# Kernel optimization log

Hardware: AMD Instinct MI355X
Metric: run time of the kernel (lower is better)

Reference implementation:

```python
import jax, jax.numpy as jnp
import numpy as np

ATT_NORM = 4.0
EPS = 1e-12

E, H, C, N = 1000000, 8, 16, 100000


def setup_inputs() -> dict:
    key = jax.random.key(0)
    k1, k2, k3, k4, k5 = jax.random.split(key, 5)
    return {
        "x": jax.random.normal(k1, (E, H, C), dtype=jnp.float32),
        "att_l": jax.random.normal(k2, (1, H, C), dtype=jnp.float32),
        "att_r": jax.random.normal(k3, (1, H, C), dtype=jnp.float32),
        "alpha": jax.random.normal(k4, (E, H, 1), dtype=jnp.float32),
        "index": jax.random.randint(k5, (E,), 0, N, dtype=jnp.int32),
        "num_nodes": N,
    }


def reference(x, att_l, att_r, alpha, index, num_nodes):
    # squared L2 norm of per-edge features: [E, H, 1]
    norm_x = jnp.sum(x * x, axis=-1, keepdims=True)
    # scatter-max per destination node: [N, H, 1]
    max_norm_seg = jax.ops.segment_max(norm_x, index, num_segments=num_nodes)
    # gather back per edge and combine: sqrt(max_norm[index] + norm_x)
    max_norm = jnp.sqrt(max_norm_seg[index] + norm_x)  # [E, H, 1]
    # norm of concatenated attention vectors: ||[att_l, att_r]|| over last dim -> [1, H, 1]
    norm_att = ATT_NORM * jnp.sqrt(
        jnp.sum(att_l * att_l, axis=-1, keepdims=True)
        + jnp.sum(att_r * att_r, axis=-1, keepdims=True)
    )
    return alpha / (norm_att * max_norm + EPS)
```

## Files before the change

kernel.cpp:

```cpp
#include <hip/hip_runtime.h>
#include <math.h>

#define EPSF 1e-12f
#define ATT_NORM_F 4.0f
#define H_DIM 8
#define C_DIM 16
#define N_NODES 100000

__global__ __launch_bounds__(256) void lip_pass1(
    const float* __restrict__ x, const int* __restrict__ index,
    float* __restrict__ norm_x, unsigned int* __restrict__ seg, int rows)
{
    int tid = blockIdx.x * blockDim.x + threadIdx.x;
    int r = tid >> 2;
    int lane = tid & 3;
    if (r >= rows) return;

    const float4* x4 = (const float4*)x;
    float4 v = x4[(size_t)r * 4 + lane];
    float s = v.x * v.x + v.y * v.y + v.z * v.z + v.w * v.w;
    s += __shfl_xor(s, 1);
    s += __shfl_xor(s, 2);

    if (lane == 0) {
        norm_x[r] = s;
        int e = r >> 3;
        int h = r & 7;
        atomicMax(&seg[(size_t)index[e] * H_DIM + h], __float_as_uint(s));
    }
}

__global__ __launch_bounds__(256) void lip_pass2(
    const float* __restrict__ norm_x, const float* __restrict__ alpha,
    const int* __restrict__ index, const unsigned int* __restrict__ seg,
    const float* __restrict__ att_l, const float* __restrict__ att_r,
    float* __restrict__ out, int total)
{
    __shared__ float s_natt[H_DIM];
    int t = threadIdx.x;
    if (t < H_DIM) {
        float s = 0.f;
        #pragma unroll
        for (int c = 0; c < C_DIM; ++c) {
            float l = att_l[t * C_DIM + c];
            float r = att_r[t * C_DIM + c];
            s += l * l + r * r;
        }
        s_natt[t] = ATT_NORM_F * sqrtf(s);
    }
    __syncthreads();

    int tid = blockIdx.x * blockDim.x + t;
    if (tid >= total) return;

    int e    = tid >> 1;
    int half = tid & 1;
    int idx  = index[e];

    const float4* nx4 = (const float4*)norm_x;
    const float4* al4 = (const float4*)alpha;
    const float4* sg4 = (const float4*)seg;

    float4 nx = nx4[tid];
    float4 al = al4[tid];
    float4 sg = sg4[(size_t)idx * 2 + half];

    int h0 = half * 4;
    float4 o;
    o.x = al.x / (s_natt[h0 + 0] * sqrtf(sg.x + nx.x) + EPSF);
    o.y = al.y / (s_natt[h0 + 1] * sqrtf(sg.y + nx.y) + EPSF);
    o.z = al.z / (s_natt[h0 + 2] * sqrtf(sg.z + nx.z) + EPSF);
    o.w = al.w / (s_natt[h0 + 3] * sqrtf(sg.w + nx.w) + EPSF);
    ((float4*)out)[tid] = o;
}

__global__ __launch_bounds__(256) void lip_pass2_recompute(
    const float* __restrict__ x, const float* __restrict__ alpha,
    const int* __restrict__ index, const unsigned int* __restrict__ seg,
    const float* __restrict__ att_l, const float* __restrict__ att_r,
    float* __restrict__ out, int rows)
{
    __shared__ float s_natt[H_DIM];
    int t = threadIdx.x;
    if (t < H_DIM) {
        float s = 0.f;
        #pragma unroll
        for (int c = 0; c < C_DIM; ++c) {
            float l = att_l[t * C_DIM + c];
            float r = att_r[t * C_DIM + c];
            s += l * l + r * r;
        }
        s_natt[t] = ATT_NORM_F * sqrtf(s);
    }
    __syncthreads();

    int r = blockIdx.x * blockDim.x + t;
    if (r >= rows) return;

    const float4* x4 = (const float4*)x;
    float s = 0.f;
    #pragma unroll
    for (int q = 0; q < 4; ++q) {
        float4 v = x4[(size_t)r * 4 + q];
        s += v.x * v.x + v.y * v.y + v.z * v.z + v.w * v.w;
    }
    int e = r >> 3;
    int h = r & 7;
    float sg = __uint_as_float(seg[(size_t)index[e] * H_DIM + h]);
    out[r] = alpha[r] / (s_natt[h] * sqrtf(sg + s) + EPSF);
}

extern "C" void kernel_launch(void* const* d_in, const int* in_sizes, int n_in,
                              void* d_out, int out_size, void* d_ws, size_t ws_size,
                              hipStream_t stream) {
    const float* x     = (const float*)d_in[0];
    const float* att_l = (const float*)d_in[1];
    const float* att_r = (const float*)d_in[2];
    const float* alpha = (const float*)d_in[3];
    const int*   index = (const int*)d_in[4];

    const int E    = in_sizes[4];
    const int rows = E * H_DIM;

    size_t seg_bytes = (size_t)N_NODES * H_DIM * sizeof(unsigned int);
    size_t seg_pad   = (seg_bytes + 255) / 256 * 256;
    size_t need      = seg_pad + (size_t)rows * sizeof(float);

    unsigned int* seg = (unsigned int*)d_ws;
    hipMemsetAsync(seg, 0, seg_bytes, stream);

    if (ws_size >= need) {
        float* norm_x = (float*)((char*)d_ws + seg_pad);
        int t1 = rows * 4;
        lip_pass1<<<(t1 + 255) / 256, 256, 0, stream>>>(x, index, norm_x, seg, rows);
        int t2 = E * 2;
        lip_pass2<<<(t2 + 255) / 256, 256, 0, stream>>>(
            norm_x, alpha, index, seg, att_l, att_r, (float*)d_out, t2);
    } else {
        int t1 = rows * 4;
        lip_pass1<<<(t1 + 255) / 256, 256, 0, stream>>>(x, index, (float*)d_out, seg, rows);
        lip_pass2_recompute<<<(rows + 255) / 256, 256, 0, stream>>>(
            x, alpha, index, seg, att_l, att_r, (float*)d_out, rows);
    }
}
```

Baseline: 154.6 us.

## Fuse both passes into persistent kernel with grid barrier and register-held norms

Replaces the two-pass scheme, which stored per-row norms to a workspace array, with one persistent kernel of 1024 blocks. Each thread computes 31 row norms, keeps them in registers, does the scatter atomicMax, waits at a software grid barrier, then gathers the segment max and writes the output. This removes the global norm_x write and read and one kernel launch, and a small zero kernel replaces hipMemsetAsync. In exchange it relies on all 1024 blocks being co-resident for the spin barrier to be safe, and it moves to row-per-thread addressing with uncoalesced x loads and scalar stores, plus heavy register use for the 31-entry array.

```diff
diff --git a/kernel.cpp b/kernel.cpp
--- a/kernel.cpp
+++ b/kernel.cpp
@@ -7,34 +7,47 @@
 #define C_DIM 16
 #define N_NODES 100000
 
-__global__ __launch_bounds__(256) void lip_pass1(
-    const float* __restrict__ x, const int* __restrict__ index,
-    float* __restrict__ norm_x, unsigned int* __restrict__ seg, int rows)
+#define TPB 256
+#define NBLK 1024
+#define NTHREADS (NBLK * TPB)
+#define ITERS 31
+
+__global__ __launch_bounds__(256) void lip_zero(unsigned* __restrict__ p, int n)
 {
-    int tid = blockIdx.x * blockDim.x + threadIdx.x;
-    int r = tid >> 2;
-    int lane = tid & 3;
-    if (r >= rows) return;
-
-    const float4* x4 = (const float4*)x;
-    float4 v = x4[(size_t)r * 4 + lane];
-    float s = v.x * v.x + v.y * v.y + v.z * v.z + v.w * v.w;
-    s += __shfl_xor(s, 1);
-    s += __shfl_xor(s, 2);
-
-    if (lane == 0) {
-        norm_x[r] = s;
-        int e = r >> 3;
-        int h = r & 7;
-        atomicMax(&seg[(size_t)index[e] * H_DIM + h], __float_as_uint(s));
-    }
+    int i = blockIdx.x * 256 + threadIdx.x;
+    if (i < n) p[i] = 0u;
 }
 
-__global__ __launch_bounds__(256) void lip_pass2(
-    const float* __restrict__ norm_x, const float* __restrict__ alpha,
-    const int* __restrict__ index, const unsigned int* __restrict__ seg,
-    const float* __restrict__ att_l, const float* __restrict__ att_r,
-    float* __restrict__ out, int total)
+__device__ __forceinline__ void grid_barrier(unsigned* bar, unsigned nblk)
+{
+    __syncthreads();
+    if (threadIdx.x == 0) {
+        __threadfence();
+        unsigned g = __hip_atomic_load(&bar[1], __ATOMIC_RELAXED,
+                                       __HIP_MEMORY_SCOPE_AGENT);
+        unsigned old = __hip_atomic_fetch_add(&bar[0], 1u, __ATOMIC_ACQ_REL,
+                                              __HIP_MEMORY_SCOPE_AGENT);
+        if (old == nblk - 1) {
+            __hip_atomic_store(&bar[0], 0u, __ATOMIC_RELAXED,
+                               __HIP_MEMORY_SCOPE_AGENT);
+            __hip_atomic_fetch_add(&bar[1], 1u, __ATOMIC_RELEASE,
+                                   __HIP_MEMORY_SCOPE_AGENT);
+        } else {
+            while (__hip_atomic_load(&bar[1], __ATOMIC_ACQUIRE,
+                                     __HIP_MEMORY_SCOPE_AGENT) == g) {
+                __builtin_amdgcn_s_sleep(2);
+            }
+        }
+        __threadfence();
+    }
+    __syncthreads();
+}
+
+__global__ __launch_bounds__(TPB, 4) void lip_fused(
+    const float* __restrict__ x, const float* __restrict__ att_l,
+    const float* __restrict__ att_r, const float* __restrict__ alpha,
+    const int* __restrict__ index, float* __restrict__ out,
+    unsigned* __restrict__ seg, unsigned* __restrict__ bar, int rows)
 {
     __shared__ float s_natt[H_DIM];
     int t = threadIdx.x;
@@ -48,30 +61,63 @@
         }
         s_natt[t] = ATT_NORM_F * sqrtf(s);
     }
-    __syncthreads();
 
-    int tid = blockIdx.x * blockDim.x + t;
-    if (tid >= total) return;
+    const int tid = blockIdx.x * TPB + t;
+    const float4* x4 = (const float4*)x;
+    float nrm[ITERS];
 
-    int e    = tid >> 1;
-    int half = tid & 1;
-    int idx  = index[e];
+    #pragma unroll
+    for (int i = 0; i < ITERS; ++i) {
+        int r = tid + i * NTHREADS;
+        nrm[i] = 0.f;
+        if (r < rows) {
+            float s = 0.f;
+            #pragma unroll
+            for (int q = 0; q < 4; ++q) {
+                float4 v = x4[(size_t)r * 4 + q];
+                s += v.x * v.x + v.y * v.y + v.z * v.z + v.w * v.w;
+            }
+            nrm[i] = s;
+            int e = r >> 3;
+            int h = r & 7;
+            atomicMax(&seg[(size_t)index[e] * H_DIM + h], __float_as_uint(s));
+        }
+    }
 
-    const float4* nx4 = (const float4*)norm_x;
-    const float4* al4 = (const float4*)alpha;
-    const float4* sg4 = (const float4*)seg;
+    grid_barrier(bar, NBLK);
 
-    float4 nx = nx4[tid];
-    float4 al = al4[tid];
-    float4 sg = sg4[(size_t)idx * 2 + half];
+    #pragma unroll
+    for (int i = 0; i < ITERS; ++i) {
+        int r = tid + i * NTHREADS;
+        if (r < rows) {
+            int e = r >> 3;
+            int h = r & 7;
+            unsigned sgb = __hip_atomic_load(
+                &seg[(size_t)index[e] * H_DIM + h],
+                __ATOMIC_RELAXED, __HIP_MEMORY_SCOPE_AGENT);
+            out[r] = alpha[r] /
+                     (s_natt[h] * sqrtf(__uint_as_float(sgb) + nrm[i]) + EPSF);
+        }
+    }
+}
 
-    int h0 = half * 4;
-    float4 o;
-    o.x = al.x / (s_natt[h0 + 0] * sqrtf(sg.x + nx.x) + EPSF);
-    o.y = al.y / (s_natt[h0 + 1] * sqrtf(sg.y + nx.y) + EPSF);
-    o.z = al.z / (s_natt[h0 + 2] * sqrtf(sg.z + nx.z) + EPSF);
-    o.w = al.w / (s_natt[h0 + 3] * sqrtf(sg.w + nx.w) + EPSF);
-    ((float4*)out)[tid] = o;
+__global__ __launch_bounds__(256) void lip_pass1(
+    const float* __restrict__ x, const int* __restrict__ index,
+    unsigned int* __restrict__ seg, int rows)
+{
+    int tid = blockIdx.x * blockDim.x + threadIdx.x;
+    int r = tid >> 2;
+    int lane = tid & 3;
+    if (r >= rows) return;
+    const float4* x4 = (const float4*)x;
+    float4 v = x4[(size_t)r * 4 + lane];
+    float s = v.x * v.x + v.y * v.y + v.z * v.z + v.w * v.w;
+    s += __shfl_xor(s, 1);
+    s += __shfl_xor(s, 2);
+    if (lane == 0) {
+        int e = r >> 3, h = r & 7;
+        atomicMax(&seg[(size_t)index[e] * H_DIM + h], __float_as_uint(s));
+    }
 }
 
 __global__ __launch_bounds__(256) void lip_pass2_recompute(
@@ -93,10 +139,8 @@
         s_natt[t] = ATT_NORM_F * sqrtf(s);
     }
     __syncthreads();
-
     int r = blockIdx.x * blockDim.x + t;
     if (r >= rows) return;
-
     const float4* x4 = (const float4*)x;
     float s = 0.f;
     #pragma unroll
@@ -104,8 +148,7 @@
         float4 v = x4[(size_t)r * 4 + q];
         s += v.x * v.x + v.y * v.y + v.z * v.z + v.w * v.w;
     }
-    int e = r >> 3;
-    int h = r & 7;
+    int e = r >> 3, h = r & 7;
     float sg = __uint_as_float(seg[(size_t)index[e] * H_DIM + h]);
     out[r] = alpha[r] / (s_natt[h] * sqrtf(sg + s) + EPSF);
 }
@@ -122,23 +165,19 @@
     const int E    = in_sizes[4];
     const int rows = E * H_DIM;
 
-    size_t seg_bytes = (size_t)N_NODES * H_DIM * sizeof(unsigned int);
-    size_t seg_pad   = (seg_bytes + 255) / 256 * 256;
-    size_t need      = seg_pad + (size_t)rows * sizeof(float);
+    const int seg_words = N_NODES * H_DIM;
+    const int zero_words = seg_words + 2;
+    unsigned* seg = (unsigned*)d_ws;
+    unsigned* bar = seg + seg_words;
 
-    unsigned int* seg = (unsigned int*)d_ws;
-    hipMemsetAsync(seg, 0, seg_bytes, stream);
-
-    if (ws_size >= need) {
-        float* norm_x = (float*)((char*)d_ws + seg_pad);
+    if (ws_size >= (size_t)zero_words * 4) {
+        lip_zero<<<(zero_words + 255) / 256, 256, 0, stream>>>(seg, zero_words);
+        lip_fused<<<NBLK, TPB, 0, stream>>>(
+            x, att_l, att_r, alpha, index, (float*)d_out, seg, bar, rows);
+    } else {
+        lip_zero<<<(seg_words + 255) / 256, 256, 0, stream>>>(seg, seg_words);
         int t1 = rows * 4;
-        lip_pass1<<<(t1 + 255) / 256, 256, 0, stream>>>(x, index, norm_x, seg, rows);
-        int t2 = E * 2;
-        lip_pass2<<<(t2 + 255) / 256, 256, 0, stream>>>(
-            norm_x, alpha, index, seg, att_l, att_r, (float*)d_out, t2);
-    } else {
-        int t1 = rows * 4;
-        lip_pass1<<<(t1 + 255) / 256, 256, 0, stream>>>(x, index, (float*)d_out, seg, rows);
+        lip_pass1<<<(t1 + 255) / 256, 256, 0, stream>>>(x, index, seg, rows);
         lip_pass2_recompute<<<(rows + 255) / 256, 256, 0, stream>>>(
             x, alpha, index, seg, att_l, att_r, (float*)d_out, rows);
     }
```

Measured after the change: 513.9 us. +232.3%, slower.
